# Optimization experiments

Hardware: AMD Instinct MI355X
Metric: run time of the kernel (lower is better)

Reference implementation:

```python
import jax, jax.numpy as jnp
import numpy as np

H = 256
N0, N1, N2 = 150000, 80000, 20000
E0, E1 = 800000, 300000


def setup_inputs() -> dict:
    key = jax.random.key(0)
    ks = jax.random.split(key, 16)
    sc = 1.0 / np.sqrt(H)
    return {
        "x": jax.random.normal(ks[0], (N0, H), jnp.float32),
        # GATConv params (heads=1): lin weight, att_src, att_dst, bias
        "W_gat": jax.random.normal(ks[1], (H, H), jnp.float32) * sc,
        "att_src": jax.random.normal(ks[2], (H,), jnp.float32) * sc,
        "att_dst": jax.random.normal(ks[3], (H,), jnp.float32) * sc,
        "b_gat": jax.random.normal(ks[4], (H,), jnp.float32) * 0.01,
        # SAGEConv layer 0: lin_l (aggregated, with bias), lin_r (root, no bias)
        "Wl0": jax.random.normal(ks[5], (H, H), jnp.float32) * sc,
        "bl0": jnp.zeros((H,), jnp.float32),
        "Wr0": jax.random.normal(ks[6], (H, H), jnp.float32) * sc,
        # SAGEConv layer 1
        "Wl1": jax.random.normal(ks[7], (H, H), jnp.float32) * sc,
        "bl1": jnp.zeros((H,), jnp.float32),
        "Wr1": jax.random.normal(ks[8], (H, H), jnp.float32) * sc,
        # NeighborSampler bipartite edge lists (src -> dst)
        "src0": jax.random.randint(ks[9], (E0,), 0, N0, dtype=jnp.int32),
        "dst0": jax.random.randint(ks[10], (E0,), 0, N1, dtype=jnp.int32),
        "src1": jax.random.randint(ks[11], (E1,), 0, N1, dtype=jnp.int32),
        "dst1": jax.random.randint(ks[12], (E1,), 0, N2, dtype=jnp.int32),
        "n1": N1,
        "n2": N2,
    }


def _gat(x, src, dst, W, a_s, a_d, b):
    """PyG GATConv, heads=1, add_self_loops=True, eval mode (dropout no-op)."""
    N = x.shape[0]
    h = x @ W                                   # [N, H]
    loops = jnp.arange(N, dtype=src.dtype)      # self loops over all N nodes
    s = jnp.concatenate([src, loops])
    d = jnp.concatenate([dst, loops])
    al_s = (h * a_s).sum(-1)                    # [N]
    al_d = (h * a_d).sum(-1)                    # [N]
    e = jax.nn.leaky_relu(al_s[s] + al_d[d], 0.2)
    m = jax.ops.segment_max(e, d, num_segments=N)     # softmax over dst groups
    w = jnp.exp(e - m[d])
    z = jax.ops.segment_sum(w, d, num_segments=N)
    coef = w / z[d]
    out = jax.ops.segment_sum(coef[:, None] * h[s], d, num_segments=N)
    return out + b


def _sage(x_src, x_tgt, src, dst, n_tgt, Wl, bl, Wr):
    """PyG SAGEConv((x, x_target), edge_index), mean aggr, normalize=True."""
    msg = x_src[src]                                         # [E, H]
    ssum = jax.ops.segment_sum(msg, dst, num_segments=n_tgt)
    cnt = jax.ops.segment_sum(jnp.ones(src.shape, msg.dtype), dst,
                              num_segments=n_tgt)
    mean = ssum / jnp.maximum(cnt, 1.0)[:, None]
    out = mean @ Wl + bl + x_tgt @ Wr
    nrm = jnp.linalg.norm(out, axis=-1, keepdims=True)       # F.normalize
    return out / jnp.maximum(nrm, 1e-12)


def reference(x, W_gat, att_src, att_dst, b_gat, Wl0, bl0, Wr0, Wl1, bl1, Wr1,
              src0, dst0, src1, dst1, n1, n2):
    # Layer 0 (its result is discarded by the original module: x = x_all each
    # iteration and only the final x is appended to xs).
    h0 = _gat(x, src0, dst0, W_gat, att_src, att_dst, b_gat)
    _ = jax.nn.relu(_sage(h0, h0[:n1], src0, dst0, n1, Wl0, bl0, Wr0))
    # Layer 1 (the returned output)
    h1 = _gat(x, src1, dst1, W_gat, att_src, att_dst, b_gat)
    out = _sage(h1, h1[:n2], src1, dst1, n2, Wl1, bl1, Wr1)
    return out
```

## Files before the change

### kernel.cpp

```cpp
#include <hip/hip_runtime.h>


#define NS 80000
#define ND 20000

typedef float   float4v  __attribute__((ext_vector_type(4)));
typedef float   f32x4    __attribute__((ext_vector_type(4)));
typedef __bf16  bf16x8   __attribute__((ext_vector_type(8)));
typedef unsigned short ushort8v __attribute__((ext_vector_type(8)));
typedef unsigned short ushort2v __attribute__((ext_vector_type(2)));
typedef int     int4v    __attribute__((ext_vector_type(4)));

union frag_u { ushort8v u; bf16x8 b; };

__device__ __forceinline__ float us2f(unsigned short u) {
    union { unsigned int i; float f; } x; x.i = ((unsigned)u) << 16; return x.f;
}
__device__ __forceinline__ unsigned short f2us(float f) {
    union { __bf16 b; unsigned short u; } x; x.b = (__bf16)f; return x.u;
}
__device__ __forceinline__ float lrelu02(float x) { return x > 0.f ? x : 0.2f * x; }

__global__ __launch_bounds__(256) void prep_misc(
    const float* __restrict__ Wg, const float* __restrict__ Wl,
    const float* __restrict__ Wr, unsigned short* __restrict__ Wgt,
    unsigned short* __restrict__ Wcat, int* __restrict__ zerop, int nz4)
{
    const int b = blockIdx.x, t = threadIdx.x;
    if (b < 256) {
        Wgt[b * 256 + t] = f2us(Wg[t * 256 + b]);
    } else if (b < 512) {
        const int n = b - 256;
        Wcat[n * 512 + t]       = f2us(Wl[t * 256 + n]);
        Wcat[n * 512 + 256 + t] = f2us(Wr[t * 256 + n]);
    } else {
        const int i = (b - 512) * 256 + t;
        if (i < nz4) ((int4v*)zerop)[i] = (int4v){0, 0, 0, 0};
    }
}

__global__ void count_rank(const int* __restrict__ src, const int* __restrict__ dst,
                           int* __restrict__ cntpair, int* __restrict__ rank, int E)
{
    const int i = blockIdx.x * 256 + threadIdx.x;
    if (i < E) {
        const int d = dst[i];
        const int cls = (src[i] < ND) ? 0 : 1;
        rank[i] = atomicAdd(&cntpair[2 * d + cls], 1);
    }
}

template <int EPI, bool AF32, bool SCAN>
__global__ __launch_bounds__(512) void gemm_mfma(
    const void* __restrict__ Av, const unsigned short* __restrict__ Bt,
    int M, int K,
    unsigned short* __restrict__ hb_out,
    const float* __restrict__ avs, const float* __restrict__ avd,
    float* __restrict__ al_s, float* __restrict__ al_d,
    const float* __restrict__ bias, float* __restrict__ outp,
    int nblk, const int* __restrict__ cntpair, int* __restrict__ ptrp)
{
    __shared__ __align__(16) unsigned short Als[2][128][40];
    __shared__ __align__(16) unsigned short Bls[2][256][40];
    __shared__ float red0[128];
    __shared__ float red1[128];

    if (SCAN && (int)blockIdx.x >= nblk) {
        int* part = (int*)Als;
        const int tid = threadIdx.x;
        const int chunk = (ND + 511) / 512;
        const int i0 = tid * chunk;
        const int i1 = min(i0 + chunk, ND);
        int s = 0;
        for (int i = i0; i < i1; ++i) s += cntpair[2*i] + cntpair[2*i+1];
        part[tid] = s;
        __syncthreads();
        for (int off = 1; off < 512; off <<= 1) {
            const int t = (tid >= off) ? part[tid - off] : 0;
            __syncthreads();
            part[tid] += t;
            __syncthreads();
        }
        int run = tid ? part[tid - 1] : 0;
        for (int i = i0; i < i1; ++i) { ptrp[i] = run; run += cntpair[2*i] + cntpair[2*i+1]; }
        if (tid == 511) ptrp[ND] = part[511];
        return;
    }

    const int tid  = threadIdx.x;
    const int lane = tid & 63;
    const int wid  = tid >> 6;
    const int wr   = wid >> 2;
    const int wc   = wid & 3;
    const int row0 = blockIdx.x * 128;
    const int lg   = lane >> 4;
    const int lm   = lane & 15;

    f32x4 acc[4][4] = {};

    const int arow = tid >> 2;
    const int akof = (tid & 3) * 8;
    const int brow = tid >> 1;
    const int bkof = (tid & 1) * 16;
    const int nk   = K >> 5;

    ushort8v avr, bvr0, bvr1;

    auto load_t = [&](int kt) {
        const int k0 = kt * 32;
        if constexpr (AF32) {
            const float* ag = (const float*)Av + (size_t)(row0 + arow) * K + k0 + akof;
            const float4v v0 = *(const float4v*)ag;
            const float4v v1 = *(const float4v*)(ag + 4);
            avr[0]=f2us(v0[0]); avr[1]=f2us(v0[1]); avr[2]=f2us(v0[2]); avr[3]=f2us(v0[3]);
            avr[4]=f2us(v1[0]); avr[5]=f2us(v1[1]); avr[6]=f2us(v1[2]); avr[7]=f2us(v1[3]);
        } else {
            if (row0 + arow < M) {
                avr = *(const ushort8v*)((const unsigned short*)Av + (size_t)(row0 + arow) * K + k0 + akof);
            } else {
                avr = (ushort8v){0,0,0,0,0,0,0,0};
            }
        }
        const unsigned short* bgp = Bt + (size_t)brow * K + k0 + bkof;
        bvr0 = *(const ushort8v*)bgp;
        bvr1 = *(const ushort8v*)(bgp + 8);
    };
    auto store_t = [&](int b) {
        *(ushort8v*)&Als[b][arow][akof]     = avr;
        *(ushort8v*)&Bls[b][brow][bkof]     = bvr0;
        *(ushort8v*)&Bls[b][brow][bkof + 8] = bvr1;
    };

    load_t(0); store_t(0); __syncthreads();
    if (nk > 1) load_t(1);
    int cur = 0;

    for (int kt = 0; kt < nk; ++kt) {
        frag_u af[4], bf[4];
#pragma unroll
        for (int m = 0; m < 4; ++m)
            af[m].u = *(const ushort8v*)&Als[cur][wr*64 + m*16 + lm][lg*8];
#pragma unroll
        for (int n = 0; n < 4; ++n)
            bf[n].u = *(const ushort8v*)&Bls[cur][wc*64 + n*16 + lm][lg*8];
#pragma unroll
        for (int m = 0; m < 4; ++m)
#pragma unroll
            for (int n = 0; n < 4; ++n)
                acc[m][n] = __builtin_amdgcn_mfma_f32_16x16x32_bf16(
                    af[m].b, bf[n].b, acc[m][n], 0, 0, 0);
        if (kt + 1 < nk) {
            store_t(cur ^ 1);
            __syncthreads();
            if (kt + 2 < nk) load_t(kt + 2);
            cur ^= 1;
        }
    }

    if constexpr (EPI == 0) {
        if (tid < 128) { red0[tid] = 0.f; red1[tid] = 0.f; }
        __syncthreads();
        float asv[4], adv[4], bgv[4];
#pragma unroll
        for (int n = 0; n < 4; ++n) {
            const int col = wc*64 + n*16 + lm;
            asv[n] = avs[col]; adv[n] = avd[col]; bgv[n] = bias[col];
        }
#pragma unroll
        for (int m = 0; m < 4; ++m) {
#pragma unroll
            for (int j = 0; j < 4; ++j) {
                const int lr = wr*64 + m*16 + lg*4 + j;
                float ps = 0.f, pd = 0.f;
#pragma unroll
                for (int n = 0; n < 4; ++n) {
                    const float v = acc[m][n][j];
                    ps += v * asv[n]; pd += v * adv[n];
                    hb_out[(size_t)(row0 + lr) * 256 + wc*64 + n*16 + lm] = f2us(v + bgv[n]);
                }
#pragma unroll
                for (int off = 1; off < 16; off <<= 1) {
                    ps += __shfl_xor(ps, off);
                    pd += __shfl_xor(pd, off);
                }
                if (lm == 0) { atomicAdd(&red0[lr], ps); atomicAdd(&red1[lr], pd); }
            }
        }
        __syncthreads();
        if (tid < 128) { al_s[row0 + tid] = red0[tid]; al_d[row0 + tid] = red1[tid]; }
    } else {
        if (tid < 128) red0[tid] = 0.f;
        __syncthreads();
        float bv[4];
#pragma unroll
        for (int n = 0; n < 4; ++n) bv[n] = bias[wc*64 + n*16 + lm];
#pragma unroll
        for (int m = 0; m < 4; ++m) {
#pragma unroll
            for (int j = 0; j < 4; ++j) {
                const int lr = wr*64 + m*16 + lg*4 + j;
                float ss = 0.f;
#pragma unroll
                for (int n = 0; n < 4; ++n) {
                    const float v = acc[m][n][j] + bv[n];
                    acc[m][n][j] = v;
                    ss += v * v;
                }
#pragma unroll
                for (int off = 1; off < 16; off <<= 1) ss += __shfl_xor(ss, off);
                if (lm == 0) atomicAdd(&red0[lr], ss);
            }
        }
        __syncthreads();
#pragma unroll
        for (int m = 0; m < 4; ++m) {
#pragma unroll
            for (int j = 0; j < 4; ++j) {
                const int lr = wr*64 + m*16 + lg*4 + j;
                const int grow = row0 + lr;
                if (grow < M) {
                    const float inv = 1.0f / fmaxf(sqrtf(red0[lr]), 1e-12f);
#pragma unroll
                    for (int n = 0; n < 4; ++n)
                        outp[(size_t)grow * 256 + wc*64 + n*16 + lm] = acc[m][n][j] * inv;
                }
            }
        }
    }
}

__global__ void edge_scatter(const int* __restrict__ src, const int* __restrict__ dst,
                             const int* __restrict__ ptrp, const int* __restrict__ rank,
                             const int* __restrict__ cntpair,
                             int* __restrict__ ssort, int E)
{
    const int i = blockIdx.x * 256 + threadIdx.x;
    if (i < E) {
        const int d = dst[i];
        const int s = src[i];
        const int base = ptrp[d];
        const int pos = (s < ND) ? base + rank[i]
                                 : base + cntpair[2 * d] + rank[i];
        ssort[pos] = s;
    }
}

__global__ __launch_bounds__(128) void gat_sage(
    const unsigned short* __restrict__ hb, const float* __restrict__ al_s,
    const float* __restrict__ al_d, const int* __restrict__ ssort,
    const int* __restrict__ ptrp, unsigned short* __restrict__ hcat)
{
    __shared__ float ldsg[4][264];
    __shared__ float ldss[4][264];
    __shared__ float zp[4];
    const int v    = blockIdx.x;
    const int tid  = threadIdx.x;
    const int slot = tid >> 5;
    const int l32  = tid & 31;
    const int c0   = l32 * 8;
    const int p0 = ptrp[v], p1 = ptrp[v + 1];

    const float ad     = al_d[v];
    const float w_self = __expf(lrelu02(al_s[v] + ad));

    float accg[8], accs[8];
    float zpart = 0.f;
#pragma unroll
    for (int j = 0; j < 8; ++j) accs[j] = 0.f;
    if (slot == 0) {
        const ushort8v hv = *(const ushort8v*)&hb[(size_t)v * 256 + c0];
#pragma unroll
        for (int j = 0; j < 8; ++j) accg[j] = w_self * us2f(hv[j]);
    } else {
#pragma unroll
        for (int j = 0; j < 8; ++j) accg[j] = 0.f;
    }

    int p = p0 + slot;
    for (; p + 4 < p1; p += 8) {
        const int s0 = ssort[p];
        const int s1 = ssort[p + 4];
        const float w0 = __expf(lrelu02(al_s[s0] + ad));
        const float w1 = __expf(lrelu02(al_s[s1] + ad));
        const ushort8v h0 = *(const ushort8v*)&hb[(size_t)s0 * 256 + c0];
        const ushort8v h1 = *(const ushort8v*)&hb[(size_t)s1 * 256 + c0];
        zpart += w0 + w1;
        const bool g0 = (s0 >= ND), g1 = (s1 >= ND);
#pragma unroll
        for (int j = 0; j < 8; ++j) {
            const float f0 = us2f(h0[j]);
            const float f1 = us2f(h1[j]);
            accg[j] = fmaf(w0, f0, accg[j]);
            accg[j] = fmaf(w1, f1, accg[j]);
            accs[j] += (g0 ? f0 : 0.f) + (g1 ? f1 : 0.f);
        }
    }
    if (p < p1) {
        const int s0 = ssort[p];
        const float w0 = __expf(lrelu02(al_s[s0] + ad));
        const ushort8v h0 = *(const ushort8v*)&hb[(size_t)s0 * 256 + c0];
        zpart += w0;
        const bool g0 = (s0 >= ND);
#pragma unroll
        for (int j = 0; j < 8; ++j) {
            const float f0 = us2f(h0[j]);
            accg[j] = fmaf(w0, f0, accg[j]);
            accs[j] += g0 ? f0 : 0.f;
        }
    }

    if (l32 == 0) zp[slot] = zpart;
    *(f32x4*)&ldsg[slot][c0]     = (f32x4){accg[0], accg[1], accg[2], accg[3]};
    *(f32x4*)&ldsg[slot][c0 + 4] = (f32x4){accg[4], accg[5], accg[6], accg[7]};
    *(f32x4*)&ldss[slot][c0]     = (f32x4){accs[0], accs[1], accs[2], accs[3]};
    *(f32x4*)&ldss[slot][c0 + 4] = (f32x4){accs[4], accs[5], accs[6], accs[7]};
    __syncthreads();

    const float inv_z = 1.0f / (w_self + zp[0] + zp[1] + zp[2] + zp[3]);
    const int c = tid * 2;
    float rg0 = 0.f, rg1 = 0.f, rs0 = 0.f, rs1 = 0.f;
#pragma unroll
    for (int s2 = 0; s2 < 4; ++s2) {
        rg0 += ldsg[s2][c];     rg1 += ldsg[s2][c + 1];
        rs0 += ldss[s2][c];     rs1 += ldss[s2][c + 1];
    }
    *(ushort2v*)&hcat[(size_t)v * 512 + 256 + c] =
        (ushort2v){f2us(rg0 * inv_z), f2us(rg1 * inv_z)};
    *(ushort2v*)&hcat[(size_t)v * 512 + c] =
        (ushort2v){f2us(rs0), f2us(rs1)};
}

__global__ __launch_bounds__(256) void sage_fin(
    const int* __restrict__ ssort, const int* __restrict__ ptrp,
    const int* __restrict__ cntpair, unsigned short* __restrict__ hcat)
{
    const int tid   = threadIdx.x;
    const int g     = tid >> 6;
    const int v     = blockIdx.x * 4 + g;
    const int slot2 = (tid >> 5) & 1;
    const int l32   = tid & 31;
    const int c0    = l32 * 8;
    const int p0  = ptrp[v];
    const int p1l = p0 + cntpair[2 * v];
    const int deg = ptrp[v + 1] - p0;

    float acc[8];
    if (slot2 == 0) {
        const ushort8v pv = *(const ushort8v*)&hcat[(size_t)v * 512 + c0];
#pragma unroll
        for (int j = 0; j < 8; ++j) acc[j] = us2f(pv[j]);
    } else {
#pragma unroll
        for (int j = 0; j < 8; ++j) acc[j] = 0.f;
    }
    int p = p0 + slot2;
    for (; p + 2 < p1l; p += 4) {
        const int s0 = ssort[p];
        const int s1 = ssort[p + 2];
        const ushort8v h0 = *(const ushort8v*)&hcat[(size_t)s0 * 512 + 256 + c0];
        const ushort8v h1 = *(const ushort8v*)&hcat[(size_t)s1 * 512 + 256 + c0];
#pragma unroll
        for (int j = 0; j < 8; ++j) acc[j] += us2f(h0[j]) + us2f(h1[j]);
    }
    if (p < p1l) {
        const int s0 = ssort[p];
        const ushort8v h0 = *(const ushort8v*)&hcat[(size_t)s0 * 512 + 256 + c0];
#pragma unroll
        for (int j = 0; j < 8; ++j) acc[j] += us2f(h0[j]);
    }
#pragma unroll
    for (int j = 0; j < 8; ++j) acc[j] += __shfl_xor(acc[j], 32);

    const float inv = (deg > 0) ? 1.0f / (float)deg : 0.f;
    if (slot2 == 0) {
        ushort8v o;
#pragma unroll
        for (int j = 0; j < 8; ++j) o[j] = f2us(acc[j] * inv);
        *(ushort8v*)&hcat[(size_t)v * 512 + c0] = o;
    }
}

extern "C" void kernel_launch(void* const* d_in, const int* in_sizes, int n_in,
                              void* d_out, int out_size, void* d_ws, size_t ws_size,
                              hipStream_t stream)
{
    const float* x    = (const float*)d_in[0];
    const float* Wg   = (const float*)d_in[1];
    const float* asrc = (const float*)d_in[2];
    const float* adst = (const float*)d_in[3];
    const float* bg   = (const float*)d_in[4];
    const float* Wl1  = (const float*)d_in[8];
    const float* bl1  = (const float*)d_in[9];
    const float* Wr1  = (const float*)d_in[10];
    const int*   src1 = (const int*)d_in[13];
    const int*   dst1 = (const int*)d_in[14];
    const int E1 = in_sizes[13];

    char* w = (char*)d_ws;
    unsigned short* hb   = (unsigned short*)w; w += (size_t)NS * 256 * 2;
    unsigned short* hcat = (unsigned short*)w; w += (size_t)ND * 512 * 2;
    unsigned short* Wgt  = (unsigned short*)w; w += 256 * 256 * 2;
    unsigned short* Wcat = (unsigned short*)w; w += 256 * 512 * 2;
    float* al_s   = (float*)w; w += (size_t)NS * 4;
    float* al_d   = (float*)w; w += (size_t)NS * 4;
    int* cntpair  = (int*)w;   w += (size_t)2 * ND * 4;
    int* ptrv     = (int*)w;   w += (size_t)(ND + 4) * 4;
    int* rank     = (int*)w;   w += (size_t)E1 * 4;
    int* ssort    = (int*)w;   w += (size_t)E1 * 4;

    const dim3 b256(256), b512(512);
    const int nz4 = 2 * ND / 4;

    prep_misc<<<dim3(512 + (nz4 + 255) / 256), b256, 0, stream>>>(
        Wg, Wl1, Wr1, Wgt, Wcat, cntpair, nz4);

    count_rank<<<dim3((E1 + 255) / 256), b256, 0, stream>>>(
        src1, dst1, cntpair, rank, E1);

    const int nblk0 = NS / 128;
    gemm_mfma<0, true, true><<<dim3(nblk0 + 1), b512, 0, stream>>>(
        x, Wgt, NS, 256, hb, asrc, adst, al_s, al_d, bg, nullptr,
        nblk0, cntpair, ptrv);

    edge_scatter<<<dim3((E1 + 255) / 256), b256, 0, stream>>>(
        src1, dst1, ptrv, rank, cntpair, ssort, E1);

    gat_sage<<<dim3(ND), dim3(128), 0, stream>>>(hb, al_s, al_d, ssort,
                                                 ptrv, hcat);
    sage_fin<<<dim3(ND / 4), b256, 0, stream>>>(ssort, ptrv, cntpair, hcat);

    gemm_mfma<1, false, false><<<dim3((ND + 127) / 128), b512, 0, stream>>>(
        hcat, Wcat, ND, 512, nullptr, nullptr, nullptr, nullptr, nullptr,
        bl1, (float*)d_out, 0, nullptr, nullptr);
}
```

Measured before the change: 144.5 us.

## Load GEMM MFMA fragments straight from global memory, dropping LDS staging

Removes the shared-memory double buffer for the A and B tiles and the per-k-step __syncthreads. Each wave now loads its MFMA fragments directly from global memory into registers, with a two-stage register ping-pong that prefetches the next k-tile. This cuts LDS traffic and barriers but loses reuse across waves, so global/L2 reads rise about fourfold. Register pressure also goes up. The loop assumes nk is even, which holds for K=256.

```diff
diff --git a/kernel.cpp b/kernel.cpp
--- a/kernel.cpp
+++ b/kernel.cpp
@@ -60,13 +60,11 @@
     const float* __restrict__ bias, float* __restrict__ outp,
     int nblk, const int* __restrict__ cntpair, int* __restrict__ ptrp)
 {
-    __shared__ __align__(16) unsigned short Als[2][128][40];
-    __shared__ __align__(16) unsigned short Bls[2][256][40];
     __shared__ float red0[128];
     __shared__ float red1[128];
+    __shared__ int   part[512];
 
     if (SCAN && (int)blockIdx.x >= nblk) {
-        int* part = (int*)Als;
         const int tid = threadIdx.x;
         const int chunk = (ND + 511) / 512;
         const int i0 = tid * chunk;
@@ -97,64 +95,62 @@
     const int lm   = lane & 15;
 
     f32x4 acc[4][4] = {};
-
-    const int arow = tid >> 2;
-    const int akof = (tid & 3) * 8;
-    const int brow = tid >> 1;
-    const int bkof = (tid & 1) * 16;
-    const int nk   = K >> 5;
-
-    ushort8v avr, bvr0, bvr1;
-
-    auto load_t = [&](int kt) {
-        const int k0 = kt * 32;
+    const int nk = K >> 5;
+
+    const int ar0 = row0 + wr*64 + lm;
+    const int bc0 = wc*64 + lm;
+    const int kof = lg * 8;
+
+    float4v raA0[4], raA1[4], raB0[4], raB1[4];
+    frag_u afA[4], bfA[4], afB[4], bfB[4];
+
+    auto loadA = [&](int kt, float4v (&r0)[4], float4v (&r1)[4], frag_u (&af)[4]) {
+        const int k = kt * 32 + kof;
+#pragma unroll
+        for (int m = 0; m < 4; ++m) {
+            const int ar = ar0 + m * 16;
+            if constexpr (AF32) {
+                const float* p = (const float*)Av + (size_t)ar * K + k;
+                r0[m] = *(const float4v*)p;
+                r1[m] = *(const float4v*)(p + 4);
+            } else {
+                if (ar < M)
+                    af[m].u = *(const ushort8v*)((const unsigned short*)Av + (size_t)ar * K + k);
+                else
+                    af[m].u = (ushort8v){0,0,0,0,0,0,0,0};
+            }
+        }
+    };
+    auto loadB = [&](int kt, frag_u (&bf)[4]) {
+        const int k = kt * 32 + kof;
+#pragma unroll
+        for (int n = 0; n < 4; ++n)
+            bf[n].u = *(const ushort8v*)(Bt + (size_t)(bc0 + n * 16) * K + k);
+    };
+    auto domfma = [&](float4v (&r0)[4], float4v (&r1)[4], frag_u (&af)[4], frag_u (&bf)[4]) {
         if constexpr (AF32) {
-            const float* ag = (const float*)Av + (size_t)(row0 + arow) * K + k0 + akof;
-            const float4v v0 = *(const float4v*)ag;
-            const float4v v1 = *(const float4v*)(ag + 4);
-            avr[0]=f2us(v0[0]); avr[1]=f2us(v0[1]); avr[2]=f2us(v0[2]); avr[3]=f2us(v0[3]);
-            avr[4]=f2us(v1[0]); avr[5]=f2us(v1[1]); avr[6]=f2us(v1[2]); avr[7]=f2us(v1[3]);
-        } else {
-            if (row0 + arow < M) {
-                avr = *(const ushort8v*)((const unsigned short*)Av + (size_t)(row0 + arow) * K + k0 + akof);
-            } else {
-                avr = (ushort8v){0,0,0,0,0,0,0,0};
+#pragma unroll
+            for (int m = 0; m < 4; ++m) {
+                af[m].u[0] = f2us(r0[m][0]); af[m].u[1] = f2us(r0[m][1]);
+                af[m].u[2] = f2us(r0[m][2]); af[m].u[3] = f2us(r0[m][3]);
+                af[m].u[4] = f2us(r1[m][0]); af[m].u[5] = f2us(r1[m][1]);
+                af[m].u[6] = f2us(r1[m][2]); af[m].u[7] = f2us(r1[m][3]);
             }
         }
-        const unsigned short* bgp = Bt + (size_t)brow * K + k0 + bkof;
-        bvr0 = *(const ushort8v*)bgp;
-        bvr1 = *(const ushort8v*)(bgp + 8);
-    };
-    auto store_t = [&](int b) {
-        *(ushort8v*)&Als[b][arow][akof]     = avr;
-        *(ushort8v*)&Bls[b][brow][bkof]     = bvr0;
-        *(ushort8v*)&Bls[b][brow][bkof + 8] = bvr1;
-    };
-
-    load_t(0); store_t(0); __syncthreads();
-    if (nk > 1) load_t(1);
-    int cur = 0;
-
-    for (int kt = 0; kt < nk; ++kt) {
-        frag_u af[4], bf[4];
-#pragma unroll
-        for (int m = 0; m < 4; ++m)
-            af[m].u = *(const ushort8v*)&Als[cur][wr*64 + m*16 + lm][lg*8];
-#pragma unroll
-        for (int n = 0; n < 4; ++n)
-            bf[n].u = *(const ushort8v*)&Bls[cur][wc*64 + n*16 + lm][lg*8];
 #pragma unroll
         for (int m = 0; m < 4; ++m)
 #pragma unroll
             for (int n = 0; n < 4; ++n)
                 acc[m][n] = __builtin_amdgcn_mfma_f32_16x16x32_bf16(
                     af[m].b, bf[n].b, acc[m][n], 0, 0, 0);
-        if (kt + 1 < nk) {
-            store_t(cur ^ 1);
-            __syncthreads();
-            if (kt + 2 < nk) load_t(kt + 2);
-            cur ^= 1;
-        }
+    };
+
+    loadA(0, raA0, raA1, afA); loadB(0, bfA);
+    for (int kt = 0; kt < nk; kt += 2) {
+        loadA(kt + 1, raB0, raB1, afB); loadB(kt + 1, bfB);
+        domfma(raA0, raA1, afA, bfA);
+        if (kt + 2 < nk) { loadA(kt + 2, raA0, raA1, afA); loadB(kt + 2, bfA); }
+        domfma(raB0, raB1, afB, bfB);
     }
 
     if constexpr (EPI == 0) {
```

Measured after the change: 191.5 us. 1.33x slower.

## Shrink GEMM row tile to 64 and drop LDS double buffering

Applied to the files above, without the earlier changes.

The MFMA GEMM now handles 64 rows per block instead of 128. Each of the 8 waves covers all 64 rows and a 32-column slice, so every block still produces all 256 output columns. The LDS double buffer becomes a single buffer: the next tile is prefetched into registers and stored after an extra barrier. The aim is more blocks (1250 for the first GEMM, 313 for the last) and less LDS per block, for better occupancy and CU fill. The cost is that the B matrix is reloaded twice as often per output row, and each K step now needs two barriers instead of one.

```diff
diff --git a/kernel.cpp b/kernel.cpp
--- a/kernel.cpp
+++ b/kernel.cpp
@@ -8,6 +8,7 @@
 typedef float   f32x4    __attribute__((ext_vector_type(4)));
 typedef __bf16  bf16x8   __attribute__((ext_vector_type(8)));
 typedef unsigned short ushort8v __attribute__((ext_vector_type(8)));
+typedef unsigned short ushort4v __attribute__((ext_vector_type(4)));
 typedef unsigned short ushort2v __attribute__((ext_vector_type(2)));
 typedef int     int4v    __attribute__((ext_vector_type(4)));
 
@@ -60,13 +61,13 @@
     const float* __restrict__ bias, float* __restrict__ outp,
     int nblk, const int* __restrict__ cntpair, int* __restrict__ ptrp)
 {
-    __shared__ __align__(16) unsigned short Als[2][128][40];
-    __shared__ __align__(16) unsigned short Bls[2][256][40];
-    __shared__ float red0[128];
-    __shared__ float red1[128];
+    __shared__ __align__(16) unsigned short Als[64][40];
+    __shared__ __align__(16) unsigned short Bls[256][40];
+    __shared__ float red0[64];
+    __shared__ float red1[64];
 
     if (SCAN && (int)blockIdx.x >= nblk) {
-        int* part = (int*)Als;
+        int* part = (int*)Bls;
         const int tid = threadIdx.x;
         const int chunk = (ND + 511) / 512;
         const int i0 = tid * chunk;
@@ -89,94 +90,92 @@
 
     const int tid  = threadIdx.x;
     const int lane = tid & 63;
-    const int wid  = tid >> 6;
-    const int wr   = wid >> 2;
-    const int wc   = wid & 3;
-    const int row0 = blockIdx.x * 128;
+    const int wc   = tid >> 6;
+    const int row0 = blockIdx.x * 64;
     const int lg   = lane >> 4;
     const int lm   = lane & 15;
 
-    f32x4 acc[4][4] = {};
-
-    const int arow = tid >> 2;
-    const int akof = (tid & 3) * 8;
+    f32x4 acc[4][2] = {};
+    const int nk = K >> 5;
+
+    const int arow = tid >> 3;
+    const int akof = (tid & 7) * 4;
     const int brow = tid >> 1;
     const int bkof = (tid & 1) * 16;
-    const int nk   = K >> 5;
-
-    ushort8v avr, bvr0, bvr1;
+
+    float4v ar;
+    ushort4v ai;
+    ushort8v bvr0, bvr1;
 
     auto load_t = [&](int kt) {
         const int k0 = kt * 32;
+        const int grow = row0 + arow;
         if constexpr (AF32) {
-            const float* ag = (const float*)Av + (size_t)(row0 + arow) * K + k0 + akof;
-            const float4v v0 = *(const float4v*)ag;
-            const float4v v1 = *(const float4v*)(ag + 4);
-            avr[0]=f2us(v0[0]); avr[1]=f2us(v0[1]); avr[2]=f2us(v0[2]); avr[3]=f2us(v0[3]);
-            avr[4]=f2us(v1[0]); avr[5]=f2us(v1[1]); avr[6]=f2us(v1[2]); avr[7]=f2us(v1[3]);
+            ar = *(const float4v*)((const float*)Av + (size_t)grow * K + k0 + akof);
         } else {
-            if (row0 + arow < M) {
-                avr = *(const ushort8v*)((const unsigned short*)Av + (size_t)(row0 + arow) * K + k0 + akof);
-            } else {
-                avr = (ushort8v){0,0,0,0,0,0,0,0};
-            }
+            if (grow < M)
+                ai = *(const ushort4v*)((const unsigned short*)Av + (size_t)grow * K + k0 + akof);
+            else
+                ai = (ushort4v){0, 0, 0, 0};
         }
         const unsigned short* bgp = Bt + (size_t)brow * K + k0 + bkof;
         bvr0 = *(const ushort8v*)bgp;
         bvr1 = *(const ushort8v*)(bgp + 8);
     };
-    auto store_t = [&](int b) {
-        *(ushort8v*)&Als[b][arow][akof]     = avr;
-        *(ushort8v*)&Bls[b][brow][bkof]     = bvr0;
-        *(ushort8v*)&Bls[b][brow][bkof + 8] = bvr1;
+    auto store_t = [&]() {
+        if constexpr (AF32) {
+            ushort4v t;
+            t[0] = f2us(ar[0]); t[1] = f2us(ar[1]);
+            t[2] = f2us(ar[2]); t[3] = f2us(ar[3]);
+            *(ushort4v*)&Als[arow][akof] = t;
+        } else {
+            *(ushort4v*)&Als[arow][akof] = ai;
+        }
+        *(ushort8v*)&Bls[brow][bkof]     = bvr0;
+        *(ushort8v*)&Bls[brow][bkof + 8] = bvr1;
     };
 
-    load_t(0); store_t(0); __syncthreads();
-    if (nk > 1) load_t(1);
-    int cur = 0;
+    load_t(0); store_t(); __syncthreads();
 
     for (int kt = 0; kt < nk; ++kt) {
-        frag_u af[4], bf[4];
+        if (kt + 1 < nk) load_t(kt + 1);
+        frag_u af[4], bf[2];
 #pragma unroll
         for (int m = 0; m < 4; ++m)
-            af[m].u = *(const ushort8v*)&Als[cur][wr*64 + m*16 + lm][lg*8];
-#pragma unroll
-        for (int n = 0; n < 4; ++n)
-            bf[n].u = *(const ushort8v*)&Bls[cur][wc*64 + n*16 + lm][lg*8];
+            af[m].u = *(const ushort8v*)&Als[m*16 + lm][lg*8];
+#pragma unroll
+        for (int n = 0; n < 2; ++n)
+            bf[n].u = *(const ushort8v*)&Bls[wc*32 + n*16 + lm][lg*8];
 #pragma unroll
         for (int m = 0; m < 4; ++m)
 #pragma unroll
-            for (int n = 0; n < 4; ++n)
+            for (int n = 0; n < 2; ++n)
                 acc[m][n] = __builtin_amdgcn_mfma_f32_16x16x32_bf16(
                     af[m].b, bf[n].b, acc[m][n], 0, 0, 0);
-        if (kt + 1 < nk) {
-            store_t(cur ^ 1);
-            __syncthreads();
-            if (kt + 2 < nk) load_t(kt + 2);
-            cur ^= 1;
-        }
+        __syncthreads();
+        if (kt + 1 < nk) { store_t(); __syncthreads(); }
     }
 
     if constexpr (EPI == 0) {
-        if (tid < 128) { red0[tid] = 0.f; red1[tid] = 0.f; }
-        __syncthreads();
-        float asv[4], adv[4], bgv[4];
-#pragma unroll
-        for (int n = 0; n < 4; ++n) {
-            const int col = wc*64 + n*16 + lm;
+        if (tid < 64) { red0[tid] = 0.f; red1[tid] = 0.f; }
+        __syncthreads();
+        float asv[2], adv[2], bgv[2];
+#pragma unroll
+        for (int n = 0; n < 2; ++n) {
+            const int col = wc*32 + n*16 + lm;
             asv[n] = avs[col]; adv[n] = avd[col]; bgv[n] = bias[col];
         }
 #pragma unroll
         for (int m = 0; m < 4; ++m) {
 #pragma unroll
             for (int j = 0; j < 4; ++j) {
-                const int lr = wr*64 + m*16 + lg*4 + j;
+                const int lr = m*16 + lg*4 + j;
                 float ps = 0.f, pd = 0.f;
 #pragma unroll
-                for (int n = 0; n < 4; ++n) {
+                for (int n = 0; n < 2; ++n) {
                     const float v = acc[m][n][j];
                     ps += v * asv[n]; pd += v * adv[n];
-                    hb_out[(size_t)(row0 + lr) * 256 + wc*64 + n*16 + lm] = f2us(v + bgv[n]);
+                    hb_out[(size_t)(row0 + lr) * 256 + wc*32 + n*16 + lm] = f2us(v + bgv[n]);
                 }
 #pragma unroll
                 for (int off = 1; off < 16; off <<= 1) {
@@ -187,21 +186,21 @@
             }
         }
         __syncthreads();
-        if (tid < 128) { al_s[row0 + tid] = red0[tid]; al_d[row0 + tid] = red1[tid]; }
+        if (tid < 64) { al_s[row0 + tid] = red0[tid]; al_d[row0 + tid] = red1[tid]; }
     } else {
-        if (tid < 128) red0[tid] = 0.f;
-        __syncthreads();
-        float bv[4];
-#pragma unroll
-        for (int n = 0; n < 4; ++n) bv[n] = bias[wc*64 + n*16 + lm];
+        if (tid < 64) red0[tid] = 0.f;
+        __syncthreads();
+        float bv[2];
+#pragma unroll
+        for (int n = 0; n < 2; ++n) bv[n] = bias[wc*32 + n*16 + lm];
 #pragma unroll
         for (int m = 0; m < 4; ++m) {
 #pragma unroll
             for (int j = 0; j < 4; ++j) {
-                const int lr = wr*64 + m*16 + lg*4 + j;
+                const int lr = m*16 + lg*4 + j;
                 float ss = 0.f;
 #pragma unroll
-                for (int n = 0; n < 4; ++n) {
+                for (int n = 0; n < 2; ++n) {
                     const float v = acc[m][n][j] + bv[n];
                     acc[m][n][j] = v;
                     ss += v * v;
@@ -216,13 +215,13 @@
         for (int m = 0; m < 4; ++m) {
 #pragma unroll
             for (int j = 0; j < 4; ++j) {
-                const int lr = wr*64 + m*16 + lg*4 + j;
+                const int lr = m*16 + lg*4 + j;
                 const int grow = row0 + lr;
                 if (grow < M) {
                     const float inv = 1.0f / fmaxf(sqrtf(red0[lr]), 1e-12f);
 #pragma unroll
-                    for (int n = 0; n < 4; ++n)
-                        outp[(size_t)grow * 256 + wc*64 + n*16 + lm] = acc[m][n][j] * inv;
+                    for (int n = 0; n < 2; ++n)
+                        outp[(size_t)grow * 256 + wc*32 + n*16 + lm] = acc[m][n][j] * inv;
                 }
             }
         }
@@ -417,7 +416,7 @@
     count_rank<<<dim3((E1 + 255) / 256), b256, 0, stream>>>(
         src1, dst1, cntpair, rank, E1);
 
-    const int nblk0 = NS / 128;
+    const int nblk0 = NS / 64;
     gemm_mfma<0, true, true><<<dim3(nblk0 + 1), b512, 0, stream>>>(
         x, Wgt, NS, 256, hb, asrc, adst, al_s, al_d, bg, nullptr,
         nblk0, cntpair, ptrv);
@@ -429,7 +428,7 @@
                                                  ptrv, hcat);
     sage_fin<<<dim3(ND / 4), b256, 0, stream>>>(ssort, ptrv, cntpair, hcat);
 
-    gemm_mfma<1, false, false><<<dim3((ND + 127) / 128), b512, 0, stream>>>(
+    gemm_mfma<1, false, false><<<dim3((ND + 63) / 64), b512, 0, stream>>>(
         hcat, Wcat, ND, 512, nullptr, nullptr, nullptr, nullptr, nullptr,
         bl1, (float*)d_out, 0, nullptr, nullptr);
 }
```

Result: slower. 154.6 us (+7.0%).

## Shrink GEMM tile to 64 rows and read B fragments directly from global

Applied to the files above, without the earlier changes.

The MFMA GEMM moves from 128-row tiles with 512 threads to 64-row tiles with 256 threads. The shared-memory staging of the weight matrix B is removed, and each wave loads its B fragments straight from global memory (L2-resident) each k-step. The A-tile prefetch now issues before the barrier, with the fp32-to-bf16 conversion deferred to the store. This cuts LDS use and raises occupancy (launch bounds 256,4) and block count. The cost is less reuse of B per block and more global/L2 traffic for weights.

```diff
diff --git a/kernel.cpp b/kernel.cpp
--- a/kernel.cpp
+++ b/kernel.cpp
@@ -51,7 +51,7 @@
 }
 
 template <int EPI, bool AF32, bool SCAN>
-__global__ __launch_bounds__(512) void gemm_mfma(
+__global__ __launch_bounds__(256, 4) void gemm_mfma(
     const void* __restrict__ Av, const unsigned short* __restrict__ Bt,
     int M, int K,
     unsigned short* __restrict__ hb_out,
@@ -60,22 +60,21 @@
     const float* __restrict__ bias, float* __restrict__ outp,
     int nblk, const int* __restrict__ cntpair, int* __restrict__ ptrp)
 {
-    __shared__ __align__(16) unsigned short Als[2][128][40];
-    __shared__ __align__(16) unsigned short Bls[2][256][40];
-    __shared__ float red0[128];
-    __shared__ float red1[128];
+    __shared__ __align__(16) unsigned short Als[2][64][40];
+    __shared__ float red0[64];
+    __shared__ float red1[64];
+    __shared__ int   part[256];
 
     if (SCAN && (int)blockIdx.x >= nblk) {
-        int* part = (int*)Als;
         const int tid = threadIdx.x;
-        const int chunk = (ND + 511) / 512;
+        const int chunk = (ND + 255) / 256;
         const int i0 = tid * chunk;
         const int i1 = min(i0 + chunk, ND);
         int s = 0;
         for (int i = i0; i < i1; ++i) s += cntpair[2*i] + cntpair[2*i+1];
         part[tid] = s;
         __syncthreads();
-        for (int off = 1; off < 512; off <<= 1) {
+        for (int off = 1; off < 256; off <<= 1) {
             const int t = (tid >= off) ? part[tid - off] : 0;
             __syncthreads();
             part[tid] += t;
@@ -83,66 +82,67 @@
         }
         int run = tid ? part[tid - 1] : 0;
         for (int i = i0; i < i1; ++i) { ptrp[i] = run; run += cntpair[2*i] + cntpair[2*i+1]; }
-        if (tid == 511) ptrp[ND] = part[511];
+        if (tid == 255) ptrp[ND] = part[255];
         return;
     }
 
     const int tid  = threadIdx.x;
     const int lane = tid & 63;
-    const int wid  = tid >> 6;
-    const int wr   = wid >> 2;
-    const int wc   = wid & 3;
-    const int row0 = blockIdx.x * 128;
+    const int wc   = tid >> 6;
+    const int row0 = blockIdx.x * 64;
     const int lg   = lane >> 4;
     const int lm   = lane & 15;
 
     f32x4 acc[4][4] = {};
+    const int nk = K >> 5;
 
     const int arow = tid >> 2;
     const int akof = (tid & 3) * 8;
-    const int brow = tid >> 1;
-    const int bkof = (tid & 1) * 16;
-    const int nk   = K >> 5;
-
-    ushort8v avr, bvr0, bvr1;
-
-    auto load_t = [&](int kt) {
-        const int k0 = kt * 32;
+
+    float4v ar0, ar1;
+    ushort8v ai;
+
+    auto loadA = [&](int kt) {
+        const int k0 = kt * 32 + akof;
+        const int grow = row0 + arow;
         if constexpr (AF32) {
-            const float* ag = (const float*)Av + (size_t)(row0 + arow) * K + k0 + akof;
-            const float4v v0 = *(const float4v*)ag;
-            const float4v v1 = *(const float4v*)(ag + 4);
-            avr[0]=f2us(v0[0]); avr[1]=f2us(v0[1]); avr[2]=f2us(v0[2]); avr[3]=f2us(v0[3]);
-            avr[4]=f2us(v1[0]); avr[5]=f2us(v1[1]); avr[6]=f2us(v1[2]); avr[7]=f2us(v1[3]);
+            const float* p = (const float*)Av + (size_t)grow * K + k0;
+            ar0 = *(const float4v*)p;
+            ar1 = *(const float4v*)(p + 4);
         } else {
-            if (row0 + arow < M) {
-                avr = *(const ushort8v*)((const unsigned short*)Av + (size_t)(row0 + arow) * K + k0 + akof);
-            } else {
-                avr = (ushort8v){0,0,0,0,0,0,0,0};
-            }
-        }
-        const unsigned short* bgp = Bt + (size_t)brow * K + k0 + bkof;
-        bvr0 = *(const ushort8v*)bgp;
-        bvr1 = *(const ushort8v*)(bgp + 8);
+            if (grow < M)
+                ai = *(const ushort8v*)((const unsigned short*)Av + (size_t)grow * K + k0);
+            else
+                ai = (ushort8v){0,0,0,0,0,0,0,0};
+        }
     };
-    auto store_t = [&](int b) {
-        *(ushort8v*)&Als[b][arow][akof]     = avr;
-        *(ushort8v*)&Bls[b][brow][bkof]     = bvr0;
-        *(ushort8v*)&Bls[b][brow][bkof + 8] = bvr1;
+    auto storeA = [&](int b) {
+        if constexpr (AF32) {
+            ushort8v t;
+            t[0] = f2us(ar0[0]); t[1] = f2us(ar0[1]); t[2] = f2us(ar0[2]); t[3] = f2us(ar0[3]);
+            t[4] = f2us(ar1[0]); t[5] = f2us(ar1[1]); t[6] = f2us(ar1[2]); t[7] = f2us(ar1[3]);
+            *(ushort8v*)&Als[b][arow][akof] = t;
+        } else {
+            *(ushort8v*)&Als[b][arow][akof] = ai;
+        }
     };
 
-    load_t(0); store_t(0); __syncthreads();
-    if (nk > 1) load_t(1);
+    loadA(0); storeA(0); __syncthreads();
+    if (nk > 1) loadA(1);
     int cur = 0;
 
     for (int kt = 0; kt < nk; ++kt) {
-        frag_u af[4], bf[4];
+        frag_u bf[4];
+        {
+            const int k = kt * 32 + lg * 8;
+#pragma unroll
+            for (int n = 0; n < 4; ++n)
+                bf[n].u = *(const ushort8v*)(Bt + (size_t)(wc*64 + n*16 + lm) * K + k);
+        }
+        frag_u af[4];
 #pragma unroll
         for (int m = 0; m < 4; ++m)
-            af[m].u = *(const ushort8v*)&Als[cur][wr*64 + m*16 + lm][lg*8];
-#pragma unroll
-        for (int n = 0; n < 4; ++n)
-            bf[n].u = *(const ushort8v*)&Bls[cur][wc*64 + n*16 + lm][lg*8];
+            af[m].u = *(const ushort8v*)&Als[cur][m*16 + lm][lg*8];
 #pragma unroll
         for (int m = 0; m < 4; ++m)
 #pragma unroll
@@ -150,15 +150,15 @@
                 acc[m][n] = __builtin_amdgcn_mfma_f32_16x16x32_bf16(
                     af[m].b, bf[n].b, acc[m][n], 0, 0, 0);
         if (kt + 1 < nk) {
-            store_t(cur ^ 1);
+            storeA(cur ^ 1);
+            if (kt + 2 < nk) loadA(kt + 2);
             __syncthreads();
-            if (kt + 2 < nk) load_t(kt + 2);
             cur ^= 1;
         }
     }
 
     if constexpr (EPI == 0) {
-        if (tid < 128) { red0[tid] = 0.f; red1[tid] = 0.f; }
+        if (tid < 64) { red0[tid] = 0.f; red1[tid] = 0.f; }
         __syncthreads();
         float asv[4], adv[4], bgv[4];
 #pragma unroll
@@ -170,7 +170,7 @@
         for (int m = 0; m < 4; ++m) {
 #pragma unroll
             for (int j = 0; j < 4; ++j) {
-                const int lr = wr*64 + m*16 + lg*4 + j;
+                const int lr = m*16 + lg*4 + j;
                 float ps = 0.f, pd = 0.f;
 #pragma unroll
                 for (int n = 0; n < 4; ++n) {
@@ -187,9 +187,9 @@
             }
         }
         __syncthreads();
-        if (tid < 128) { al_s[row0 + tid] = red0[tid]; al_d[row0 + tid] = red1[tid]; }
+        if (tid < 64) { al_s[row0 + tid] = red0[tid]; al_d[row0 + tid] = red1[tid]; }
     } else {
-        if (tid < 128) red0[tid] = 0.f;
+        if (tid < 64) red0[tid] = 0.f;
         __syncthreads();
         float bv[4];
 #pragma unroll
@@ -198,7 +198,7 @@
         for (int m = 0; m < 4; ++m) {
 #pragma unroll
             for (int j = 0; j < 4; ++j) {
-                const int lr = wr*64 + m*16 + lg*4 + j;
+                const int lr = m*16 + lg*4 + j;
                 float ss = 0.f;
 #pragma unroll
                 for (int n = 0; n < 4; ++n) {
@@ -216,7 +216,7 @@
         for (int m = 0; m < 4; ++m) {
 #pragma unroll
             for (int j = 0; j < 4; ++j) {
-                const int lr = wr*64 + m*16 + lg*4 + j;
+                const int lr = m*16 + lg*4 + j;
                 const int grow = row0 + lr;
                 if (grow < M) {
                     const float inv = 1.0f / fmaxf(sqrtf(red0[lr]), 1e-12f);
@@ -408,7 +408,7 @@
     int* rank     = (int*)w;   w += (size_t)E1 * 4;
     int* ssort    = (int*)w;   w += (size_t)E1 * 4;
 
-    const dim3 b256(256), b512(512);
+    const dim3 b256(256);
     const int nz4 = 2 * ND / 4;
 
     prep_misc<<<dim3(512 + (nz4 + 255) / 256), b256, 0, stream>>>(
@@ -417,8 +417,8 @@
     count_rank<<<dim3((E1 + 255) / 256), b256, 0, stream>>>(
         src1, dst1, cntpair, rank, E1);
 
-    const int nblk0 = NS / 128;
-    gemm_mfma<0, true, true><<<dim3(nblk0 + 1), b512, 0, stream>>>(
+    const int nblk0 = NS / 64;
+    gemm_mfma<0, true, true><<<dim3(nblk0 + 1), b256, 0, stream>>>(
         x, Wgt, NS, 256, hb, asrc, adst, al_s, al_d, bg, nullptr,
         nblk0, cntpair, ptrv);
 
@@ -429,7 +429,7 @@
                                                  ptrv, hcat);
     sage_fin<<<dim3(ND / 4), b256, 0, stream>>>(ssort, ptrv, cntpair, hcat);
 
-    gemm_mfma<1, false, false><<<dim3((ND + 127) / 128), b512, 0, stream>>>(
+    gemm_mfma<1, false, false><<<dim3((ND + 63) / 64), b256, 0, stream>>>(
         hcat, Wcat, ND, 512, nullptr, nullptr, nullptr, nullptr, nullptr,
         bl1, (float*)d_out, 0, nullptr, nullptr);
 }
```

Result: slower. 152.5 us (+5.5%).
